# Kernel tuning notes

Measured on AMD Instinct MI355X. Metric: run time of the kernel, lower is better.

Reference implementation:

```python
import jax, jax.numpy as jnp
import numpy as np

NUM_HEADS = 8
HEAD_SIZE = 64
INPUT = 512
OUT = NUM_HEADS * HEAD_SIZE
B, S = 4, 2048


def setup_inputs() -> dict:
    key = jax.random.key(0)
    ks = jax.random.split(key, 6)
    return {
        "key": jax.random.normal(ks[0], (B, S, INPUT), dtype=jnp.float32),
        "key_mask": jnp.zeros((B, 1, 1, S), dtype=jnp.float32),
        "query": jax.random.normal(ks[1], (B, S, INPUT), dtype=jnp.float32),
        "value": jax.random.normal(ks[2], (B, S, INPUT), dtype=jnp.float32),
        "wq": jax.random.normal(ks[3], (INPUT, OUT), dtype=jnp.float32) * (INPUT ** -0.5),
        "wk": jax.random.normal(ks[4], (INPUT, OUT), dtype=jnp.float32) * (INPUT ** -0.5),
        "wv": jax.random.normal(ks[5], (INPUT, OUT), dtype=jnp.float32) * (INPUT ** -0.5),
    }


def _split_heads(x):
    # [B, S, H*hd] -> [B, H, S, hd]
    b, s, _ = x.shape
    return x.reshape(b, s, NUM_HEADS, HEAD_SIZE).transpose(0, 2, 1, 3)


def reference(key, key_mask, query, value, wq, wk, wv):
    q = _split_heads(query @ wq)   # [B,H,S,hd]
    k = _split_heads(key @ wk)
    v = _split_heads(value @ wv)
    scale = 1.0 / jnp.sqrt(jnp.asarray(HEAD_SIZE, q.dtype))
    logits = jnp.einsum('bhqd,bhkd->bhqk', q, k) * scale + key_mask
    attn = jax.nn.softmax(logits, axis=-1)
    out = jnp.einsum('bhqk,bhkd->bhqd', attn, v)  # [B,H,S,hd]
    out = out.transpose(0, 2, 1, 3).reshape(out.shape[0], out.shape[2], OUT)
    return out
```

## Files before the change

kernel.cpp:

```cpp
#include <hip/hip_runtime.h>

typedef _Float16 f16;
typedef f16 f16x8 __attribute__((ext_vector_type(8)));
typedef f16 f16x4 __attribute__((ext_vector_type(4)));
typedef f16 f16x2 __attribute__((ext_vector_type(2)));
typedef float f32x4 __attribute__((ext_vector_type(4)));
typedef float f32x16 __attribute__((ext_vector_type(16)));
typedef unsigned int u32;
typedef u32 u32x2 __attribute__((ext_vector_type(2)));
typedef u32 u32x4 __attribute__((ext_vector_type(4)));

#define MFMA16(a, b, c) __builtin_amdgcn_mfma_f32_16x16x32_f16(a, b, c, 0, 0, 0)
#define MFMA32(a, b, c) __builtin_amdgcn_mfma_f32_32x32x16_f16(a, b, c, 0, 0, 0)

#define BATCH 4
#define NHEADS 8
#define HDIM 64
#define SEQ 2048
#define DIN 512
#define DOUT 512
#define LOG2E 1.44269504f
#define C1 0.18033688f

__device__ __forceinline__ void gl_lds16(const void* g, const void* l) {
  __builtin_amdgcn_global_load_lds(
      (const __attribute__((address_space(1))) u32*)g,
      (__attribute__((address_space(3))) u32*)l, 16, 0, 0);
}

__device__ __forceinline__ float fexp2(float x) {
  float r;
  asm("v_exp_f32 %0, %1" : "=v"(r) : "v"(x));
  return r;
}

__device__ __forceinline__ u32 pk2u(float a, float b) {
  return __builtin_bit_cast(u32, __builtin_amdgcn_cvt_pkrtz(a, b));
}

__device__ __forceinline__ f16x2 pk2(float a, float b) {
  return __builtin_bit_cast(f16x2, __builtin_amdgcn_cvt_pkrtz(a, b));
}

__device__ __forceinline__ f16x4 pk4(float a, float b, float c, float d) {
  f16x2 u0 = pk2(a, b), u1 = pk2(c, d);
  f16x4 r;
  r[0] = u0[0]; r[1] = u0[1]; r[2] = u1[0]; r[3] = u1[1];
  return r;
}

__global__ __launch_bounds__(256) void prep_w(
    const float* __restrict__ wq, const float* __restrict__ wk,
    const float* __restrict__ wv, f16* __restrict__ wT) {
  __shared__ float tile[64][65];
  const float* w = blockIdx.z == 0 ? wq : (blockIdx.z == 1 ? wk : wv);
  f16* out = wT + (size_t)blockIdx.z * DIN * DOUT;
  int k0 = blockIdx.x * 64, n0 = blockIdx.y * 64;
  int t = threadIdx.x;
  int c = t & 63, rb = t >> 6;
#pragma unroll
  for (int ph = 0; ph < 16; ++ph) {
    int r = ph * 4 + rb;
    tile[r][c] = w[(size_t)(k0 + r) * DOUT + n0 + c];
  }
  __syncthreads();
#pragma unroll
  for (int ph = 0; ph < 16; ++ph) {
    int n = ph * 4 + rb;
    out[(size_t)(n0 + n) * DIN + k0 + c] = (f16)tile[c][n];
  }
}

__global__ __launch_bounds__(256, 3) void qkv_gemm(
    const float* __restrict__ xq, const float* __restrict__ xk,
    const float* __restrict__ xv, const f16* __restrict__ wT,
    f16* __restrict__ Qo, f16* __restrict__ Ko, f16* __restrict__ Vt) {
  __shared__ __attribute__((aligned(16))) f16 smem[16384];
  f16* As = smem;
  f16* Bs = smem + 8192;
  f16* CT = smem;

  int gemm = blockIdx.z;
  const float* x = gemm == 0 ? xq : (gemm == 1 ? xk : xv);
  const f16* wt = wT + (size_t)gemm * DIN * DOUT;
  int bx = blockIdx.x;
  int m0 = (bx & 63) * 128, n0 = (bx >> 6) * 128;
  int t = threadIdx.x, w = t >> 6, lane = t & 63;
  int lr = lane & 15, lq = lane >> 4;
  int wm = (w >> 1) * 64, wn = (w & 1) * 64;

  int tr = t >> 4, tc = t & 15;
  const float* xg = x + (size_t)(m0 + tr) * DIN + tc * 4;
  int aw[8];
#pragma unroll
  for (int ph = 0; ph < 8; ++ph) {
    int r = tr + 16 * ph;
    int phys = (tc >> 1) ^ (r & 7);
    aw[ph] = r * 64 + phys * 8 + (tc & 1) * 4;
  }

  int srow = lane >> 3;
  int schunk = (lane & 7) ^ srow;
  const f16* gb[4];
  const f16* lbb[4];
#pragma unroll
  for (int j = 0; j < 4; ++j) {
    int br = w * 32 + j * 8;
    gb[j] = wt + (size_t)(n0 + br + srow) * DIN + schunk * 8;
    lbb[j] = &Bs[__builtin_amdgcn_readfirstlane(br * 64)];
  }
  int xo0 = ((0 * 4 + lq) ^ (lr & 7)) * 8;
  int xo1 = ((1 * 4 + lq) ^ (lr & 7)) * 8;

  f32x4 zero = {0.f, 0.f, 0.f, 0.f};
  f32x4 acc[4][4];
#pragma unroll
  for (int i = 0; i < 4; ++i)
#pragma unroll
    for (int j = 0; j < 4; ++j) acc[i][j] = zero;

  for (int k0 = 0; k0 < DIN; k0 += 64) {
    __syncthreads();
#pragma unroll
    for (int j = 0; j < 4; ++j) gl_lds16(gb[j] + k0, lbb[j]);
#pragma unroll
    for (int ph = 0; ph < 8; ++ph) {
      float4 a = *(const float4*)(xg + (size_t)ph * 16 * DIN + k0);
      *(f16x4*)&As[aw[ph]] = pk4(a.x, a.y, a.z, a.w);
    }
    __syncthreads();
#pragma unroll
    for (int c = 0; c < 2; ++c) {
      int xo = c ? xo1 : xo0;
      f16x8 xf[4], wf[4];
#pragma unroll
      for (int i = 0; i < 4; ++i)
        xf[i] = *(const f16x8*)&As[(wm + i * 16 + lr) * 64 + xo];
#pragma unroll
      for (int i = 0; i < 4; ++i)
        wf[i] = *(const f16x8*)&Bs[(wn + i * 16 + lr) * 64 + xo];
      if (gemm == 2) {
#pragma unroll
        for (int i = 0; i < 4; ++i)
#pragma unroll
          for (int j = 0; j < 4; ++j)
            acc[i][j] = MFMA16(xf[i], wf[j], acc[i][j]);
      } else {
#pragma unroll
        for (int i = 0; i < 4; ++i)
#pragma unroll
          for (int j = 0; j < 4; ++j)
            acc[i][j] = MFMA16(wf[i], xf[j], acc[i][j]);
      }
    }
  }

  __syncthreads();
  int b_ = m0 >> 11;
  int sl = m0 & 2047;

  if (gemm == 2) {
#pragma unroll
    for (int i = 0; i < 4; ++i) {
#pragma unroll
      for (int j = 0; j < 4; ++j) {
        int d = wn + j * 16 + lr;
        int lc = (wm >> 3) + i * 2 + (lq >> 1);
        int phys = lc ^ lr;
        *(f16x4*)&CT[d * 128 + phys * 8 + (lq & 1) * 4] =
            pk4(acc[i][j][0], acc[i][j][1], acc[i][j][2], acc[i][j][3]);
      }
    }
    __syncthreads();
    int tid16 = t & 15;
#pragma unroll
    for (int ph = 0; ph < 8; ++ph) {
      int d = ph * 16 + (t >> 4);
      int phys = tid16 ^ (d & 15);
      f16x8 vv = *(const f16x8*)&CT[d * 128 + phys * 8];
      int hgl = (n0 + d) >> 6, dd = (n0 + d) & 63;
      *(f16x8*)&Vt[(((size_t)b_ * NHEADS + hgl) * HDIM + dd) * SEQ + sl +
                   tid16 * 8] = vv;
    }
  } else {
    f16* O = gemm == 0 ? Qo : Ko;
    float sc = gemm == 0 ? C1 : 1.0f;
#pragma unroll
    for (int i = 0; i < 4; ++i) {
#pragma unroll
      for (int j = 0; j < 4; ++j) {
        int s = wm + j * 16 + lr;
        int lc = (wn >> 3) + i * 2 + (lq >> 1);
        int phys = lc ^ lr;
        *(f16x4*)&CT[s * 128 + phys * 8 + (lq & 1) * 4] =
            pk4(acc[i][j][0] * sc, acc[i][j][1] * sc, acc[i][j][2] * sc,
                acc[i][j][3] * sc);
      }
    }
    __syncthreads();
    int tid8 = t & 7;
    int hh = (t >> 3) & 1;
#pragma unroll
    for (int ph = 0; ph < 8; ++ph) {
      int s = ph * 16 + (t >> 4);
      int lc = hh * 8 + tid8;
      int phys = lc ^ (s & 15);
      f16x8 vv = *(const f16x8*)&CT[s * 128 + phys * 8];
      int hgl = (n0 >> 6) + hh;
      *(f16x8*)&O[(((size_t)b_ * NHEADS + hgl) * SEQ + sl + s) * HDIM +
                  tid8 * 8] = vv;
    }
  }
}

__global__ __launch_bounds__(256, 2) void flash_attn(
    const f16* __restrict__ Q, const f16* __restrict__ K,
    const f16* __restrict__ Vt, const float* __restrict__ mask,
    float* __restrict__ out) {
  __shared__ __attribute__((aligned(16))) f16 Ks[2 * 128 * 64];
  __shared__ __attribute__((aligned(16))) f16 Vs[2 * 64 * 128];
  __shared__ __attribute__((aligned(16))) float Ms[SEQ];

  int bh = blockIdx.x, q0 = blockIdx.y * 128;
  int b = bh >> 3, h = bh & 7;
  int t = threadIdx.x, w = t >> 6, lane = t & 63;
  int l5 = lane & 31, hf = lane >> 5;

  const f16* Qg = Q + (size_t)bh * SEQ * HDIM;
  const f16* Kg = K + (size_t)bh * SEQ * HDIM;
  const f16* Vg = Vt + (size_t)bh * HDIM * SEQ;
  const float* mg = mask + (size_t)b * SEQ;

  int krow = lane >> 3;
  int kchunk = (lane & 7) ^ krow;
  const f16* gk[4];
  const f16* gv[4];
  const f16* lk[4];
  const f16* lv[4];
#pragma unroll
  for (int j = 0; j < 4; ++j) {
    int kbr = w * 32 + j * 8;
    gk[j] = Kg + (size_t)(kbr + krow) * HDIM + kchunk * 8;
    lk[j] = &Ks[__builtin_amdgcn_readfirstlane(kbr * 64)];
    int vbr = w * 16 + j * 4;
    int lq = lane >> 4;
    int vchunk = (lane & 15) ^ ((vbr + lq) & 15);
    gv[j] = Vg + (size_t)(vbr + lq) * SEQ + vchunk * 8;
    lv[j] = &Vs[__builtin_amdgcn_readfirstlane(vbr * 128)];
  }

  {
    int c0 = w * 512;
    gl_lds16(mg + c0 + lane * 4, &Ms[__builtin_amdgcn_readfirstlane(c0)]);
    gl_lds16(mg + c0 + 256 + lane * 4,
             &Ms[__builtin_amdgcn_readfirstlane(c0 + 256)]);
  }
#pragma unroll
  for (int j = 0; j < 4; ++j) {
    gl_lds16(gk[j], lk[j]);
    gl_lds16(gv[j], lv[j]);
  }

  f16x8 qf[4];
#pragma unroll
  for (int ds = 0; ds < 4; ++ds)
    qf[ds] = *(const f16x8*)(Qg + (size_t)(q0 + w * 32 + l5) * HDIM + ds * 16 +
                             hf * 8);

  const f32x16 Z = {0.f, 0.f, 0.f, 0.f, 0.f, 0.f, 0.f, 0.f,
                    0.f, 0.f, 0.f, 0.f, 0.f, 0.f, 0.f, 0.f};
  f32x16 acc[2][2];
#pragma unroll
  for (int dt = 0; dt < 2; ++dt)
#pragma unroll
    for (int par = 0; par < 2; ++par) acc[dt][par] = Z;
  float lsum = 0.f;

  asm volatile("s_waitcnt vmcnt(0)" ::: "memory");
  __builtin_amdgcn_sched_barrier(0);
  __builtin_amdgcn_s_barrier();
  __builtin_amdgcn_sched_barrier(0);

#define QKT(nt, sv)                                                          \
  {                                                                          \
    __builtin_amdgcn_s_setprio(1);                                           \
    f16x8 kf0 = *(const f16x8*)&Kb[((nt)*32 + l5) * 64 +                     \
                                   (((0 + hf) ^ (l5 & 7)) * 8)];             \
    sv = MFMA32(kf0, qf[0], Z);                                              \
    _Pragma("unroll") for (int ds = 1; ds < 4; ++ds) {                       \
      f16x8 kf = *(const f16x8*)&Kb[((nt)*32 + l5) * 64 +                    \
                                    (((ds * 2 + hf) ^ (l5 & 7)) * 8)];       \
      sv = MFMA32(kf, qf[ds], sv);                                           \
    }                                                                        \
    __builtin_amdgcn_s_setprio(0);                                           \
  }

#define SM(nt, sv)                                                           \
  _Pragma("unroll") for (int run = 0; run < 4; ++run) {                      \
    float4 mk = *(const float4*)&Ms[k0 + (nt)*32 + run * 8 + 4 * hf];        \
    float p0 = fexp2(fmaf(mk.x, LOG2E, sv[run * 4 + 0]));                    \
    float p1 = fexp2(fmaf(mk.y, LOG2E, sv[run * 4 + 1]));                    \
    float p2 = fexp2(fmaf(mk.z, LOG2E, sv[run * 4 + 2]));                    \
    float p3 = fexp2(fmaf(mk.w, LOG2E, sv[run * 4 + 3]));                    \
    lsum += (p0 + p1) + (p2 + p3);                                           \
    pk_[nt][run][0] = pk2u(p0, p1);                                          \
    pk_[nt][run][1] = pk2u(p2, p3);                                          \
  }

  for (int it = 0; it < 16; ++it) {
    int p = it & 1;
    int k0 = it * 128;
    const f16* Kb = &Ks[p * 8192];
    const f16* Vb = &Vs[p * 8192];

    if (it < 15) {
      int pn = p ^ 1;
#pragma unroll
      for (int j = 0; j < 4; ++j) {
        gl_lds16(gk[j] + (size_t)(k0 + 128) * HDIM, lk[j] + pn * 8192);
        gl_lds16(gv[j] + k0 + 128, lv[j] + pn * 8192);
      }
    }

    u32 pk_[4][4][2];

    {
      f32x16 sA, sB;
      QKT(0, sA);
      QKT(1, sB);
      SM(0, sA);
      QKT(2, sA);
      SM(1, sB);
      QKT(3, sB);
      SM(2, sA);
      SM(3, sB);
    }

    __builtin_amdgcn_s_setprio(1);
#pragma unroll
    for (int ks = 0; ks < 8; ++ks) {
      const int nt = ks >> 1;
      const int ge = 2 * (ks & 1);
      const int go = 2 * (ks & 1) + 1;
      u32x2 r0 = __builtin_amdgcn_permlane32_swap(pk_[nt][ge][0],
                                                  pk_[nt][go][0], false, false);
      u32x2 r1 = __builtin_amdgcn_permlane32_swap(pk_[nt][ge][1],
                                                  pk_[nt][go][1], false, false);
      u32x4 apw = {r0[0], r1[0], r0[1], r1[1]};
      f16x8 ap = __builtin_bit_cast(f16x8, apw);
#pragma unroll
      for (int dt = 0; dt < 2; ++dt) {
        f16x8 bv = *(const f16x8*)&Vb[(dt * 32 + l5) * 128 +
                                      (((ks * 2 + hf) ^ (l5 & 15)) * 8)];
        acc[dt][ks & 1] = MFMA32(ap, bv, acc[dt][ks & 1]);
      }
    }
    __builtin_amdgcn_s_setprio(0);

    asm volatile("s_waitcnt vmcnt(0)" ::: "memory");
    __builtin_amdgcn_sched_barrier(0);
    __builtin_amdgcn_s_barrier();
    __builtin_amdgcn_sched_barrier(0);
  }
#undef QKT
#undef SM

  float l = lsum + __shfl_xor(lsum, 32);
  float inv = 1.f / l;
  Ms[w * 32 + l5] = inv;
  asm volatile("s_waitcnt lgkmcnt(0)" ::: "memory");
  __builtin_amdgcn_sched_barrier(0);
  float ivq[16];
#pragma unroll
  for (int r = 0; r < 16; ++r)
    ivq[r] = Ms[w * 32 + (r & 3) + 8 * (r >> 2) + 4 * hf];

#pragma unroll
  for (int dt = 0; dt < 2; ++dt) {
#pragma unroll
    for (int r = 0; r < 16; ++r) {
      int q = q0 + w * 32 + (r & 3) + 8 * (r >> 2) + 4 * hf;
      int d = h * HDIM + dt * 32 + l5;
      out[((size_t)b * SEQ + q) * DOUT + d] =
          (acc[dt][0][r] + acc[dt][1][r]) * ivq[r];
    }
  }
}

extern "C" void kernel_launch(void* const* d_in, const int* in_sizes, int n_in,
                              void* d_out, int out_size, void* d_ws,
                              size_t ws_size, hipStream_t stream) {
  const float* key = (const float*)d_in[0];
  const float* key_mask = (const float*)d_in[1];
  const float* query = (const float*)d_in[2];
  const float* value = (const float*)d_in[3];
  const float* wq = (const float*)d_in[4];
  const float* wk = (const float*)d_in[5];
  const float* wv = (const float*)d_in[6];
  float* out = (float*)d_out;

  char* ws = (char*)d_ws;
  f16* Qws = (f16*)(ws);
  f16* Kws = (f16*)(ws + 8388608);
  f16* Vtws = (f16*)(ws + 16777216);
  f16* wT = (f16*)(ws + 25165824);

  prep_w<<<dim3(8, 8, 3), 256, 0, stream>>>(wq, wk, wv, wT);
  qkv_gemm<<<dim3(256, 1, 3), 256, 0, stream>>>(query, key, value, wT, Qws,
                                                Kws, Vtws);
  flash_attn<<<dim3(32, 16), 256, 0, stream>>>(Qws, Kws, Vtws, key_mask, out);
}
```

Measured before the change: 178.9 us.

## Double-buffer weight tiles in QKV GEMM and prefetch next K-slice asynchronously

The QKV projection GEMM now keeps two LDS buffers for the weight tile, issuing the direct global-to-LDS loads for the next K step while the current step computes. Activation loads for the current step are issued into registers first, followed by an explicit vmcnt wait and raw barriers in place of __syncthreads. The goal is to hide weight-load latency behind the MFMA work. In exchange, LDS use grows from 32KB to 48KB per block, which may lower occupancy against the launch bound of 3, and the hand-written waitcnt counts must match the instruction order exactly to stay correct.

```diff
diff --git a/kernel.cpp b/kernel.cpp
--- a/kernel.cpp
+++ b/kernel.cpp
@@ -75,7 +75,7 @@
     const float* __restrict__ xq, const float* __restrict__ xk,
     const float* __restrict__ xv, const f16* __restrict__ wT,
     f16* __restrict__ Qo, f16* __restrict__ Ko, f16* __restrict__ Vt) {
-  __shared__ __attribute__((aligned(16))) f16 smem[16384];
+  __shared__ __attribute__((aligned(16))) f16 smem[24576];
   f16* As = smem;
   f16* Bs = smem + 8192;
   f16* CT = smem;
@@ -119,16 +119,31 @@
 #pragma unroll
     for (int j = 0; j < 4; ++j) acc[i][j] = zero;
 
+#pragma unroll
+  for (int j = 0; j < 4; ++j) gl_lds16(gb[j], lbb[j]);
+
   for (int k0 = 0; k0 < DIN; k0 += 64) {
-    __syncthreads();
-#pragma unroll
-    for (int j = 0; j < 4; ++j) gl_lds16(gb[j] + k0, lbb[j]);
-#pragma unroll
-    for (int ph = 0; ph < 8; ++ph) {
-      float4 a = *(const float4*)(xg + (size_t)ph * 16 * DIN + k0);
-      *(f16x4*)&As[aw[ph]] = pk4(a.x, a.y, a.z, a.w);
-    }
-    __syncthreads();
+    int p = (k0 >> 6) & 1;
+    float4 a[8];
+#pragma unroll
+    for (int ph = 0; ph < 8; ++ph)
+      a[ph] = *(const float4*)(xg + (size_t)ph * 16 * DIN + k0);
+    __builtin_amdgcn_sched_barrier(0);
+    if (k0 + 64 < DIN) {
+#pragma unroll
+      for (int j = 0; j < 4; ++j)
+        gl_lds16(gb[j] + k0 + 64, lbb[j] + ((p ^ 1) * 8192));
+    }
+    __builtin_amdgcn_sched_barrier(0);
+#pragma unroll
+    for (int ph = 0; ph < 8; ++ph)
+      *(f16x4*)&As[aw[ph]] = pk4(a[ph].x, a[ph].y, a[ph].z, a[ph].w);
+    asm volatile("s_waitcnt vmcnt(4) lgkmcnt(0)" ::: "memory");
+    __builtin_amdgcn_sched_barrier(0);
+    __builtin_amdgcn_s_barrier();
+    __builtin_amdgcn_sched_barrier(0);
+
+    const f16* Bp = Bs + p * 8192;
 #pragma unroll
     for (int c = 0; c < 2; ++c) {
       int xo = c ? xo1 : xo0;
@@ -138,7 +153,7 @@
         xf[i] = *(const f16x8*)&As[(wm + i * 16 + lr) * 64 + xo];
 #pragma unroll
       for (int i = 0; i < 4; ++i)
-        wf[i] = *(const f16x8*)&Bs[(wn + i * 16 + lr) * 64 + xo];
+        wf[i] = *(const f16x8*)&Bp[(wn + i * 16 + lr) * 64 + xo];
       if (gemm == 2) {
 #pragma unroll
         for (int i = 0; i < 4; ++i)
@@ -153,9 +168,11 @@
             acc[i][j] = MFMA16(wf[i], xf[j], acc[i][j]);
       }
     }
-  }
-
-  __syncthreads();
+    __builtin_amdgcn_sched_barrier(0);
+    __builtin_amdgcn_s_barrier();
+    __builtin_amdgcn_sched_barrier(0);
+  }
+
   int b_ = m0 >> 11;
   int sl = m0 & 2047;
 
```

New measurement: 191.7 us. 1.07x slower.
